# Kernel tuning notes

Measured on AMD Instinct MI355X. Metric: run time of the kernel, lower is better.

Reference implementation:

```python
import jax, jax.numpy as jnp
import numpy as np

B, T, D, H = 128, 365, 32, 512


def setup_inputs() -> dict:
    key = jax.random.key(0)
    k_x, k_wx, k_wh, k_b = jax.random.split(key, 4)
    scale_x = 1.0 / np.sqrt(D)
    scale_h = 1.0 / np.sqrt(H)
    x = jax.random.normal(k_x, (B, T, D), dtype=jnp.float32)
    Wx = jax.random.normal(k_wx, (D, 4 * H), dtype=jnp.float32) * scale_x  # kernel, gate order i,f,g,o
    Wh = jax.random.normal(k_wh, (H, 4 * H), dtype=jnp.float32) * scale_h  # recurrent kernel
    b = jax.random.normal(k_b, (4 * H,), dtype=jnp.float32) * 0.01
    # Keras unit_forget_bias: forget-gate bias initialized to 1
    b = b.at[H:2 * H].add(1.0)
    return {"x": x, "Wx": Wx, "Wh": Wh, "b": b}


def _lstm_seq(x, Wx, Wh, b):
    # Precompute input projections for all timesteps: [B,T,4H]
    xW = jnp.einsum("btd,dg->btg", x, Wx) + b
    h0 = jnp.zeros((x.shape[0], H), dtype=x.dtype)
    c0 = jnp.zeros((x.shape[0], H), dtype=x.dtype)

    def step(carry, xw_t):
        h, c = carry
        z = xw_t + h @ Wh  # [B,4H]
        i = jax.nn.sigmoid(z[:, 0 * H:1 * H])
        f = jax.nn.sigmoid(z[:, 1 * H:2 * H])
        g = jnp.tanh(z[:, 2 * H:3 * H])
        o = jax.nn.sigmoid(z[:, 3 * H:4 * H])
        c_new = f * c + i * g
        h_new = o * jnp.tanh(c_new)
        return (h_new, c_new), h_new

    (_, _), hs = jax.lax.scan(step, (h0, c0), jnp.swapaxes(xW, 0, 1))  # hs: [T,B,H]
    return jnp.swapaxes(hs, 0, 1)  # [B,T,H]


def reference(x, Wx, Wh, b):
    # Dense layer output is discarded in the original call(); return h sequence.
    return _lstm_seq(x, Wx, Wh, b)
```

## Files before the change

### kernel.cpp

```cpp
#include <hip/hip_runtime.h>
#include <hip/hip_fp16.h>
#include <cmath>

#define BB 128
#define TT 365
#define DD 32
#define HH 512
#define G4H 2048


typedef float f32x4 __attribute__((ext_vector_type(4)));
typedef _Float16 f16x8 __attribute__((ext_vector_type(8)));

__device__ __forceinline__ float sigf(float z) { return 1.f / (1.f + __expf(-z)); }

__device__ __forceinline__ float ftanh(float z) {
  float a = fabsf(z);
  float e = __expf(-2.f * a);
  float r = (1.f - e) / (1.f + e);
  return (z < 0.f) ? -r : r;
}

__global__ __launch_bounds__(512, 2)
void lstm_persistent(const float* __restrict__ x,
                     const float* __restrict__ Wx,
                     const float* __restrict__ Wh,
                     const float* __restrict__ bias,
                     float* __restrict__ out,
                     float* __restrict__ hws) {
  __shared__ __align__(16) _Float16 WlH[128 * 552];
  __shared__ __align__(16) _Float16 AshH[8 * 552];
  __shared__ __align__(16) float ZxS[8 * 128];
  __shared__ __align__(16) float Cs[8][32];
  __shared__ __align__(16) float BiasS[128];

  const int tid = threadIdx.x;
  const int lane = tid & 63;
  const int wv = tid >> 6;
  const int fcol = wv * 16 + (lane & 15);
  const int kq = lane >> 4;
  const int arow = lane & 15;
  const int wg = blockIdx.x;
  const int bb = wg & 15;
  const int nb = wg >> 4;
  const int b0g = bb * 8;
  const int n0 = nb * 32;

  {
    const int cl = tid & 31;
    const int pg = tid >> 5;
    for (int it = 0; it < 136; ++it) {
      int p = it * 16 + pg;
      int k = p >> 2, g = p & 3;
      int col = g * HH + n0 + cl;
      float v = (k < DD) ? Wx[k * G4H + col] : Wh[(k - DD) * G4H + col];
      WlH[(g * 32 + cl) * 552 + k] = (_Float16)v;
    }
  }
  if (tid < 128) BiasS[tid] = bias[(tid >> 5) * HH + n0 + (tid & 31)];
  if (tid < 256) Cs[tid >> 5][tid & 31] = 0.f;

  _Float16* hb0 = (_Float16*)hws;
  _Float16* hb1 = (_Float16*)(hws + BB * HH);
  unsigned int* bar = (unsigned int*)(hws + 2 * BB * HH) + bb * 32;

  __syncthreads();

  f16x8 bfrag[17];
#pragma unroll
  for (int kk = 0; kk < 17; ++kk)
    bfrag[kk] = *(const f16x8*)&WlH[fcol * 552 + kk * 32 + kq * 8];
  const float bias_r = BiasS[fcol];

  if (tid < 256) {
    int r = tid >> 5, c = tid & 31;
    AshH[r * 552 + c] = (_Float16)x[((size_t)(b0g + r) * TT + 0) * DD + c];
  }

  for (int t = 0; t < TT; ++t) {
    const _Float16* hprev = (t & 1) ? hb1 : hb0;
    _Float16* hnext = (t & 1) ? hb0 : hb1;

    if (t > 0) {
      unsigned target = 16u * (unsigned)t;
      unsigned cur;
      do {
        unsigned v = 0;
        if (lane == 0)
          v = __hip_atomic_load(bar, __ATOMIC_RELAXED,
                                __HIP_MEMORY_SCOPE_AGENT);
        cur = (unsigned)__shfl((int)v, 0);
      } while (cur < target);
    }

    unsigned long long pre[2];
#pragma unroll
    for (int r = 0; r < 2; ++r) {
      int idx = r * 512 + tid;
      int rr = idx >> 7, kk = idx & 127;
      pre[r] = __hip_atomic_load(
          (const unsigned long long*)(hprev + (size_t)(b0g + rr) * HH + kk * 4),
          __ATOMIC_RELAXED, __HIP_MEMORY_SCOPE_AGENT);
    }
#pragma unroll
    for (int r = 0; r < 2; ++r) {
      int idx = r * 512 + tid;
      int rr = idx >> 7, kk = idx & 127;
      *(unsigned long long*)&AshH[rr * 552 + DD + kk * 4] = pre[r];
    }
    __syncthreads();

    f32x4 acc0 = {bias_r, bias_r, bias_r, bias_r};
    f32x4 acc1 = {0.f, 0.f, 0.f, 0.f};
#pragma unroll
    for (int kk = 0; kk < 17; ++kk) {
      f16x8 af;
      if (arow < 8) {
        af = *(const f16x8*)&AshH[arow * 552 + kk * 32 + kq * 8];
      } else {
        f16x8 z = {};
        af = z;
      }
      if (kk & 1)
        acc1 = __builtin_amdgcn_mfma_f32_16x16x32_f16(af, bfrag[kk], acc1, 0, 0, 0);
      else
        acc0 = __builtin_amdgcn_mfma_f32_16x16x32_f16(af, bfrag[kk], acc0, 0, 0, 0);
    }
    if (kq < 2) {
#pragma unroll
      for (int r = 0; r < 4; ++r)
        ZxS[(kq * 4 + r) * 128 + fcol] = acc0[r] + acc1[r];
    }
    __syncthreads();

    float hv = 0.f;
    int bg = 0, col = 0;
    if (tid < 256) {
      int b_l = tid >> 5, nn = tid & 31;
      float zi = ZxS[b_l * 128 + nn];
      float zf = ZxS[b_l * 128 + 32 + nn];
      float zg = ZxS[b_l * 128 + 64 + nn];
      float zo = ZxS[b_l * 128 + 96 + nn];
      float cnew = sigf(zf) * Cs[b_l][nn] + sigf(zi) * ftanh(zg);
      Cs[b_l][nn] = cnew;
      hv = sigf(zo) * ftanh(cnew);
      bg = b0g + b_l;
      col = n0 + nn;
      int base = lane & ~3;
      float h0 = __shfl(hv, base + 0);
      float h1 = __shfl(hv, base + 1);
      float h2 = __shfl(hv, base + 2);
      float h3 = __shfl(hv, base + 3);
      if ((lane & 3) == 0) {
        union { unsigned long long u; _Float16 h[4]; } pk;
        pk.h[0] = (_Float16)h0;
        pk.h[1] = (_Float16)h1;
        pk.h[2] = (_Float16)h2;
        pk.h[3] = (_Float16)h3;
        __hip_atomic_store(
            (unsigned long long*)(hnext + (size_t)bg * HH + col), pk.u,
            __ATOMIC_RELAXED, __HIP_MEMORY_SCOPE_AGENT);
      }
    }
    if (t + 1 < TT && tid < 256) {
      int r = tid >> 5, c = tid & 31;
      AshH[r * 552 + c] =
          (_Float16)x[((size_t)(b0g + r) * TT + (t + 1)) * DD + c];
    }
    __syncthreads();

    if (tid == 0) {
      __hip_atomic_fetch_add(bar, 1u, __ATOMIC_RELAXED,
                             __HIP_MEMORY_SCOPE_AGENT);
    }
    if (tid < 256) {
      out[((size_t)bg * TT + t) * HH + col] = hv;
    }
  }
}

__global__ __launch_bounds__(256, 2)
void lstm_step(const float* __restrict__ x, const float* __restrict__ Wx,
               const float* __restrict__ Wh, const float* __restrict__ bias,
               float* __restrict__ out, const float* __restrict__ hprev,
               float* __restrict__ hnext, float* __restrict__ cst, int t) {
  __shared__ float Wl[16 * 544];
  __shared__ float Ash[32 * 128];
  __shared__ float Xs[32 * 32];
  __shared__ float Zx[4][32][4];
  __shared__ float BiasS[16];

  const int tid = threadIdx.x;
  const int ks = tid & 7;
  const int btile = (tid >> 3) & 7;
  const int ctile = tid >> 6;
  const int wg = blockIdx.x;
  const int bb = wg & 3;
  const int nb = wg >> 2;
  const int b0g = bb * 32;
  const int n0 = nb * 4;

  for (int idx = tid; idx < 16 * 544; idx += 256) {
    int zc = idx & 15, k = idx >> 4;
    int col = (zc >> 2) * HH + n0 + (zc & 3);
    Wl[zc * 544 + k] = (k < DD) ? Wx[k * G4H + col] : Wh[(k - DD) * G4H + col];
  }
  if (tid < 16) BiasS[tid] = bias[(tid >> 2) * HH + n0 + (tid & 3)];

  {
    int b_l = tid >> 3, kq = tid & 7;
    float4 v = *(const float4*)(x + ((size_t)(b0g + b_l) * TT + t) * DD + kq * 4);
    *(float4*)&Xs[b_l * 32 + kq * 4] = v;
  }

  float acc[4][4];
#pragma unroll
  for (int i = 0; i < 4; ++i)
#pragma unroll
    for (int c = 0; c < 4; ++c) acc[i][c] = 0.f;

  auto mac4 = [&](const float* Abase, int rstride, const float* Wbase) {
    float4 a4[4], w4[4];
#pragma unroll
    for (int i = 0; i < 4; ++i)
      a4[i] = *(const float4*)(Abase + (btile * 4 + i) * rstride);
#pragma unroll
    for (int c = 0; c < 4; ++c) w4[c] = *(const float4*)(Wbase + c * 544);
#pragma unroll
    for (int i = 0; i < 4; ++i)
#pragma unroll
      for (int c = 0; c < 4; ++c)
        acc[i][c] += a4[i].x * w4[c].x + a4[i].y * w4[c].y +
                     a4[i].z * w4[c].z + a4[i].w * w4[c].w;
  };

  for (int ch = 0; ch < 4; ++ch) {
    __syncthreads();
    for (int r = 0; r < 4; ++r) {
      int fidx = r * 256 + tid;
      int b_l = fidx >> 5, kq = fidx & 31;
      float4 v = *(const float4*)(hprev + (size_t)(b0g + b_l) * HH + ch * 128 +
                                  kq * 4);
      *(float4*)&Ash[b_l * 128 + kq * 4] = v;
    }
    __syncthreads();
    if (ch == 0) mac4(&Xs[ks * 4], 32, &Wl[(ctile * 4) * 544 + ks * 4]);
#pragma unroll
    for (int j = 0; j < 4; ++j)
      mac4(&Ash[j * 32 + ks * 4], 128,
           &Wl[(ctile * 4) * 544 + DD + ch * 128 + j * 32 + ks * 4]);
  }

#pragma unroll
  for (int i = 0; i < 4; ++i)
#pragma unroll
    for (int c = 0; c < 4; ++c) {
      float v = acc[i][c];
      v += __shfl_xor(v, 1);
      v += __shfl_xor(v, 2);
      v += __shfl_xor(v, 4);
      acc[i][c] = v;
    }

  if (ks == 0) {
#pragma unroll
    for (int i = 0; i < 4; ++i)
#pragma unroll
      for (int c = 0; c < 4; ++c)
        Zx[ctile][btile * 4 + i][c] = acc[i][c] + BiasS[ctile * 4 + c];
  }
  __syncthreads();

  if (tid < 128) {
    int b_l = tid >> 2, nn = tid & 3;
    float zi = Zx[0][b_l][nn], zf = Zx[1][b_l][nn];
    float zg = Zx[2][b_l][nn], zo = Zx[3][b_l][nn];
    int bg = b0g + b_l, col = n0 + nn;
    size_t cidx = (size_t)bg * HH + col;
    float cnew = sigf(zf) * cst[cidx] + sigf(zi) * tanhf(zg);
    cst[cidx] = cnew;
    float hv = sigf(zo) * tanhf(cnew);
    hnext[cidx] = hv;
    out[((size_t)bg * TT + t) * HH + col] = hv;
  }
}

extern "C" void kernel_launch(void* const* d_in, const int* in_sizes, int n_in,
                              void* d_out, int out_size, void* d_ws, size_t ws_size,
                              hipStream_t stream) {
  const float* x = (const float*)d_in[0];
  const float* Wx = (const float*)d_in[1];
  const float* Wh = (const float*)d_in[2];
  const float* bv = (const float*)d_in[3];
  float* out = (float*)d_out;
  float* hws = (float*)d_ws;

  hipMemsetAsync(d_ws, 0, (size_t)(3 * 65536 + 256) * 4, stream);

  void* args[] = {(void*)&x, (void*)&Wx, (void*)&Wh,
                  (void*)&bv, (void*)&out, (void*)&hws};
  hipError_t err = hipLaunchCooperativeKernel(
      reinterpret_cast<void*>(lstm_persistent), dim3(256), dim3(512), args, 0,
      stream);
  if (err != hipSuccess) {
    (void)hipGetLastError();
    float* buf0 = hws;
    float* buf1 = hws + BB * HH;
    float* cst = hws + 2 * BB * HH + 256;
    for (int t = 0; t < TT; ++t) {
      const float* hp = (t & 1) ? buf1 : buf0;
      float* hn = (t & 1) ? buf0 : buf1;
      lstm_step<<<dim3(512), dim3(256), 0, stream>>>(x, Wx, Wh, bv, out, hp, hn,
                                                     cst, t);
    }
  }
}
```

Baseline: 1.098 ms.

## Replace counter barrier with tagged h-state flags and register-level gate math

Drops the per-batch-group atomic counter barrier. Each 8-byte h packet now carries a 2-bit timestep tag in the low mantissa bits of two fp16 values, and consumers spin on the packets they read, so the separate flag round-trip goes away. The MFMA output columns are remapped so the four gates of one hidden unit sit in adjacent lanes. The cell update then runs in registers through lane shuffles, which removes the ZxS/Cs shared buffers and one __syncthreads per step. The cost is the precision lost by overwriting two mantissa bits of h, and reliance on 64-bit atomic store/load being seen as a single unit.

```diff
diff --git a/kernel.cpp b/kernel.cpp
--- a/kernel.cpp
+++ b/kernel.cpp
@@ -30,14 +30,12 @@
                      float* __restrict__ hws) {
   __shared__ __align__(16) _Float16 WlH[128 * 552];
   __shared__ __align__(16) _Float16 AshH[8 * 552];
-  __shared__ __align__(16) float ZxS[8 * 128];
-  __shared__ __align__(16) float Cs[8][32];
-  __shared__ __align__(16) float BiasS[128];
 
   const int tid = threadIdx.x;
   const int lane = tid & 63;
   const int wv = tid >> 6;
-  const int fcol = wv * 16 + (lane & 15);
+  const int g = lane & 3;
+  const int hj_loc = (lane >> 2) & 3;
   const int kq = lane >> 4;
   const int arow = lane & 15;
   const int wg = blockIdx.x;
@@ -51,26 +49,29 @@
     const int pg = tid >> 5;
     for (int it = 0; it < 136; ++it) {
       int p = it * 16 + pg;
-      int k = p >> 2, g = p & 3;
-      int col = g * HH + n0 + cl;
+      int k = p >> 2, gg = p & 3;
+      int col = gg * HH + n0 + cl;
       float v = (k < DD) ? Wx[k * G4H + col] : Wh[(k - DD) * G4H + col];
-      WlH[(g * 32 + cl) * 552 + k] = (_Float16)v;
-    }
-  }
-  if (tid < 128) BiasS[tid] = bias[(tid >> 5) * HH + n0 + (tid & 31)];
-  if (tid < 256) Cs[tid >> 5][tid & 31] = 0.f;
+      WlH[(gg * 32 + cl) * 552 + k] = (_Float16)v;
+    }
+  }
 
   _Float16* hb0 = (_Float16*)hws;
   _Float16* hb1 = (_Float16*)(hws + BB * HH);
-  unsigned int* bar = (unsigned int*)(hws + 2 * BB * HH) + bb * 32;
 
   __syncthreads();
 
+  const int colidx = g * 32 + wv * 4 + hj_loc;
   f16x8 bfrag[17];
 #pragma unroll
   for (int kk = 0; kk < 17; ++kk)
-    bfrag[kk] = *(const f16x8*)&WlH[fcol * 552 + kk * 32 + kq * 8];
-  const float bias_r = BiasS[fcol];
+    bfrag[kk] = *(const f16x8*)&WlH[colidx * 552 + kk * 32 + kq * 8];
+  const float bias_r = bias[g * HH + n0 + wv * 4 + hj_loc];
+
+  const int rr0 = tid >> 7, kk0 = tid & 127;
+  const int rr1 = (512 + tid) >> 7, kk1 = (512 + tid) & 127;
+
+  float c_st[4] = {0.f, 0.f, 0.f, 0.f};
 
   if (tid < 256) {
     int r = tid >> 5, c = tid & 31;
@@ -81,32 +82,26 @@
     const _Float16* hprev = (t & 1) ? hb1 : hb0;
     _Float16* hnext = (t & 1) ? hb0 : hb1;
 
-    if (t > 0) {
-      unsigned target = 16u * (unsigned)t;
-      unsigned cur;
-      do {
-        unsigned v = 0;
-        if (lane == 0)
-          v = __hip_atomic_load(bar, __ATOMIC_RELAXED,
-                                __HIP_MEMORY_SCOPE_AGENT);
-        cur = (unsigned)__shfl((int)v, 0);
-      } while (cur < target);
-    }
-
-    unsigned long long pre[2];
-#pragma unroll
-    for (int r = 0; r < 2; ++r) {
-      int idx = r * 512 + tid;
-      int rr = idx >> 7, kk = idx & 127;
-      pre[r] = __hip_atomic_load(
-          (const unsigned long long*)(hprev + (size_t)(b0g + rr) * HH + kk * 4),
-          __ATOMIC_RELAXED, __HIP_MEMORY_SCOPE_AGENT);
-    }
-#pragma unroll
-    for (int r = 0; r < 2; ++r) {
-      int idx = r * 512 + tid;
-      int rr = idx >> 7, kk = idx & 127;
-      *(unsigned long long*)&AshH[rr * 552 + DD + kk * 4] = pre[r];
+    {
+      const unsigned exp_tag = (unsigned)t & 3u;
+      const unsigned long long M = 0x10001ULL;
+      const unsigned long long want =
+          (unsigned long long)(exp_tag & 1u) |
+          ((unsigned long long)((exp_tag >> 1) & 1u) << 16);
+      const unsigned long long* a0 =
+          (const unsigned long long*)(hprev + (size_t)(b0g + rr0) * HH + kk0 * 4);
+      const unsigned long long* a1 =
+          (const unsigned long long*)(hprev + (size_t)(b0g + rr1) * HH + kk1 * 4);
+      unsigned long long w0 =
+          __hip_atomic_load(a0, __ATOMIC_RELAXED, __HIP_MEMORY_SCOPE_AGENT);
+      unsigned long long w1 =
+          __hip_atomic_load(a1, __ATOMIC_RELAXED, __HIP_MEMORY_SCOPE_AGENT);
+      while ((w0 & M) != want)
+        w0 = __hip_atomic_load(a0, __ATOMIC_RELAXED, __HIP_MEMORY_SCOPE_AGENT);
+      while ((w1 & M) != want)
+        w1 = __hip_atomic_load(a1, __ATOMIC_RELAXED, __HIP_MEMORY_SCOPE_AGENT);
+      *(unsigned long long*)&AshH[rr0 * 552 + DD + kk0 * 4] = w0;
+      *(unsigned long long*)&AshH[rr1 * 552 + DD + kk1 * 4] = w1;
     }
     __syncthreads();
 
@@ -126,55 +121,57 @@
       else
         acc0 = __builtin_amdgcn_mfma_f32_16x16x32_f16(af, bfrag[kk], acc0, 0, 0, 0);
     }
-    if (kq < 2) {
-#pragma unroll
-      for (int r = 0; r < 4; ++r)
-        ZxS[(kq * 4 + r) * 128 + fcol] = acc0[r] + acc1[r];
+
+    float hv[4] = {0.f, 0.f, 0.f, 0.f};
+#pragma unroll
+    for (int r = 0; r < 4; ++r) {
+      float z = acc0[r] + acc1[r];
+      float x1 = __shfl_xor(z, 1);
+      float x2 = __shfl_xor(z, 2);
+      float x3 = __shfl_xor(z, 3);
+      if (g == 0 && kq < 2) {
+        float cnew = sigf(x1) * c_st[r] + sigf(z) * ftanh(x2);
+        c_st[r] = cnew;
+        hv[r] = sigf(x3) * ftanh(cnew);
+      }
+    }
+
+    {
+      const unsigned ntag = (unsigned)(t + 1) & 3u;
+      const unsigned long long tagbits =
+          (unsigned long long)(ntag & 1u) |
+          ((unsigned long long)((ntag >> 1) & 1u) << 16);
+      const int gbase = lane & 48;
+#pragma unroll
+      for (int r = 0; r < 4; ++r) {
+        float b0 = __shfl(hv[r], gbase + 0);
+        float b1 = __shfl(hv[r], gbase + 4);
+        float b2 = __shfl(hv[r], gbase + 8);
+        float b3 = __shfl(hv[r], gbase + 12);
+        if (g == 0 && hj_loc == r && kq < 2) {
+          int row = kq * 4 + r;
+          int bg = b0g + row;
+          int col = n0 + wv * 4;
+          union { unsigned long long u; _Float16 h[4]; } pk;
+          pk.h[0] = (_Float16)b0;
+          pk.h[1] = (_Float16)b1;
+          pk.h[2] = (_Float16)b2;
+          pk.h[3] = (_Float16)b3;
+          pk.u = (pk.u & ~0x10001ULL) | tagbits;
+          __hip_atomic_store(
+              (unsigned long long*)(hnext + (size_t)bg * HH + col), pk.u,
+              __ATOMIC_RELAXED, __HIP_MEMORY_SCOPE_AGENT);
+          f32x4 ov = {b0, b1, b2, b3};
+          *(f32x4*)&out[((size_t)bg * TT + t) * HH + col] = ov;
+        }
+      }
     }
     __syncthreads();
 
-    float hv = 0.f;
-    int bg = 0, col = 0;
-    if (tid < 256) {
-      int b_l = tid >> 5, nn = tid & 31;
-      float zi = ZxS[b_l * 128 + nn];
-      float zf = ZxS[b_l * 128 + 32 + nn];
-      float zg = ZxS[b_l * 128 + 64 + nn];
-      float zo = ZxS[b_l * 128 + 96 + nn];
-      float cnew = sigf(zf) * Cs[b_l][nn] + sigf(zi) * ftanh(zg);
-      Cs[b_l][nn] = cnew;
-      hv = sigf(zo) * ftanh(cnew);
-      bg = b0g + b_l;
-      col = n0 + nn;
-      int base = lane & ~3;
-      float h0 = __shfl(hv, base + 0);
-      float h1 = __shfl(hv, base + 1);
-      float h2 = __shfl(hv, base + 2);
-      float h3 = __shfl(hv, base + 3);
-      if ((lane & 3) == 0) {
-        union { unsigned long long u; _Float16 h[4]; } pk;
-        pk.h[0] = (_Float16)h0;
-        pk.h[1] = (_Float16)h1;
-        pk.h[2] = (_Float16)h2;
-        pk.h[3] = (_Float16)h3;
-        __hip_atomic_store(
-            (unsigned long long*)(hnext + (size_t)bg * HH + col), pk.u,
-            __ATOMIC_RELAXED, __HIP_MEMORY_SCOPE_AGENT);
-      }
-    }
     if (t + 1 < TT && tid < 256) {
       int r = tid >> 5, c = tid & 31;
       AshH[r * 552 + c] =
           (_Float16)x[((size_t)(b0g + r) * TT + (t + 1)) * DD + c];
-    }
-    __syncthreads();
-
-    if (tid == 0) {
-      __hip_atomic_fetch_add(bar, 1u, __ATOMIC_RELAXED,
-                             __HIP_MEMORY_SCOPE_AGENT);
-    }
-    if (tid < 256) {
-      out[((size_t)bg * TT + t) * HH + col] = hv;
     }
   }
 }
```

New measurement: 2.148 ms. 1.96x slower.

## Replace global counter barrier with tag bits embedded in h-state words

Applied to the files above, without the earlier changes.

Drops the per-step atomic counter barrier between blocks. Each 64-bit packed fp16 h word now carries a 2-bit step tag in the mantissa LSBs of two halves, and consumers spin directly on the words they need until the tag matches. This removes the extra syncthreads, the fetch_add and the counter polling from the recurrence's critical path. The cost is corrupting the lowest mantissa bit of two h values per word, and the x load now sits inside the step.

```diff
diff --git a/kernel.cpp b/kernel.cpp
--- a/kernel.cpp
+++ b/kernel.cpp
@@ -62,7 +62,6 @@
 
   _Float16* hb0 = (_Float16*)hws;
   _Float16* hb1 = (_Float16*)(hws + BB * HH);
-  unsigned int* bar = (unsigned int*)(hws + 2 * BB * HH) + bb * 32;
 
   __syncthreads();
 
@@ -72,41 +71,38 @@
     bfrag[kk] = *(const f16x8*)&WlH[fcol * 552 + kk * 32 + kq * 8];
   const float bias_r = BiasS[fcol];
 
-  if (tid < 256) {
-    int r = tid >> 5, c = tid & 31;
-    AshH[r * 552 + c] = (_Float16)x[((size_t)(b0g + r) * TT + 0) * DD + c];
-  }
+  const int rr0 = tid >> 7, kk0 = tid & 127;
+  const int rr1 = (512 + tid) >> 7, kk1 = (512 + tid) & 127;
 
   for (int t = 0; t < TT; ++t) {
     const _Float16* hprev = (t & 1) ? hb1 : hb0;
     _Float16* hnext = (t & 1) ? hb0 : hb1;
 
-    if (t > 0) {
-      unsigned target = 16u * (unsigned)t;
-      unsigned cur;
-      do {
-        unsigned v = 0;
-        if (lane == 0)
-          v = __hip_atomic_load(bar, __ATOMIC_RELAXED,
-                                __HIP_MEMORY_SCOPE_AGENT);
-        cur = (unsigned)__shfl((int)v, 0);
-      } while (cur < target);
-    }
-
-    unsigned long long pre[2];
-#pragma unroll
-    for (int r = 0; r < 2; ++r) {
-      int idx = r * 512 + tid;
-      int rr = idx >> 7, kk = idx & 127;
-      pre[r] = __hip_atomic_load(
-          (const unsigned long long*)(hprev + (size_t)(b0g + rr) * HH + kk * 4),
-          __ATOMIC_RELAXED, __HIP_MEMORY_SCOPE_AGENT);
-    }
-#pragma unroll
-    for (int r = 0; r < 2; ++r) {
-      int idx = r * 512 + tid;
-      int rr = idx >> 7, kk = idx & 127;
-      *(unsigned long long*)&AshH[rr * 552 + DD + kk * 4] = pre[r];
+    if (tid < 256) {
+      int r = tid >> 5, c = tid & 31;
+      AshH[r * 552 + c] = (_Float16)x[((size_t)(b0g + r) * TT + t) * DD + c];
+    }
+
+    {
+      const unsigned exp_tag = (unsigned)t & 3u;
+      const unsigned long long M = 0x0000000000010001ULL;
+      const unsigned long long want =
+          (unsigned long long)(exp_tag & 1u) |
+          ((unsigned long long)((exp_tag >> 1) & 1u) << 16);
+      const unsigned long long* a0 =
+          (const unsigned long long*)(hprev + (size_t)(b0g + rr0) * HH + kk0 * 4);
+      const unsigned long long* a1 =
+          (const unsigned long long*)(hprev + (size_t)(b0g + rr1) * HH + kk1 * 4);
+      unsigned long long w0 =
+          __hip_atomic_load(a0, __ATOMIC_RELAXED, __HIP_MEMORY_SCOPE_AGENT);
+      unsigned long long w1 =
+          __hip_atomic_load(a1, __ATOMIC_RELAXED, __HIP_MEMORY_SCOPE_AGENT);
+      while ((w0 & M) != want)
+        w0 = __hip_atomic_load(a0, __ATOMIC_RELAXED, __HIP_MEMORY_SCOPE_AGENT);
+      while ((w1 & M) != want)
+        w1 = __hip_atomic_load(a1, __ATOMIC_RELAXED, __HIP_MEMORY_SCOPE_AGENT);
+      *(unsigned long long*)&AshH[rr0 * 552 + DD + kk0 * 4] = w0;
+      *(unsigned long long*)&AshH[rr1 * 552 + DD + kk1 * 4] = w1;
     }
     __syncthreads();
 
@@ -133,8 +129,6 @@
     }
     __syncthreads();
 
-    float hv = 0.f;
-    int bg = 0, col = 0;
     if (tid < 256) {
       int b_l = tid >> 5, nn = tid & 31;
       float zi = ZxS[b_l * 128 + nn];
@@ -143,37 +137,28 @@
       float zo = ZxS[b_l * 128 + 96 + nn];
       float cnew = sigf(zf) * Cs[b_l][nn] + sigf(zi) * ftanh(zg);
       Cs[b_l][nn] = cnew;
-      hv = sigf(zo) * ftanh(cnew);
-      bg = b0g + b_l;
-      col = n0 + nn;
+      float hv = sigf(zo) * ftanh(cnew);
+      int bg = b0g + b_l, col = n0 + nn;
       int base = lane & ~3;
       float h0 = __shfl(hv, base + 0);
       float h1 = __shfl(hv, base + 1);
       float h2 = __shfl(hv, base + 2);
       float h3 = __shfl(hv, base + 3);
       if ((lane & 3) == 0) {
+        const unsigned ntag = (unsigned)(t + 1) & 3u;
+        const unsigned long long tagbits =
+            (unsigned long long)(ntag & 1u) |
+            ((unsigned long long)((ntag >> 1) & 1u) << 16);
         union { unsigned long long u; _Float16 h[4]; } pk;
         pk.h[0] = (_Float16)h0;
         pk.h[1] = (_Float16)h1;
         pk.h[2] = (_Float16)h2;
         pk.h[3] = (_Float16)h3;
+        pk.u = (pk.u & ~0x0000000000010001ULL) | tagbits;
         __hip_atomic_store(
             (unsigned long long*)(hnext + (size_t)bg * HH + col), pk.u,
             __ATOMIC_RELAXED, __HIP_MEMORY_SCOPE_AGENT);
       }
-    }
-    if (t + 1 < TT && tid < 256) {
-      int r = tid >> 5, c = tid & 31;
-      AshH[r * 552 + c] =
-          (_Float16)x[((size_t)(b0g + r) * TT + (t + 1)) * DD + c];
-    }
-    __syncthreads();
-
-    if (tid == 0) {
-      __hip_atomic_fetch_add(bar, 1u, __ATOMIC_RELAXED,
-                             __HIP_MEMORY_SCOPE_AGENT);
-    }
-    if (tid < 256) {
       out[((size_t)bg * TT + t) * HH + col] = hv;
     }
   }
```

Measured after the change: 1.213 ms. 1.11x slower.
